# Performance work log

Hardware: AMD Instinct MI355X
Metric: run time of the kernel (lower is better)

The kernel has to match this reference:

```python
import jax, jax.numpy as jnp
import numpy as np

LN_EPS = 1e-12
NEG_INF = -1e9


def setup_inputs() -> dict:
    key = jax.random.key(0)
    ks = jax.random.split(key, 4)
    B, S, H = 8, 2048, 1024
    inputs = jax.random.normal(ks[0], (B, S, H), dtype=jnp.float32)
    masks = jnp.ones((B, S), dtype=jnp.int32)
    scale = 1.0 / np.sqrt(H)
    Wq = jax.random.normal(ks[1], (H, H), dtype=jnp.float32) * scale
    bq = jnp.zeros((H,), dtype=jnp.float32)
    Wk = jax.random.normal(ks[2], (H, H), dtype=jnp.float32) * scale
    bk = jnp.zeros((H,), dtype=jnp.float32)
    ln_gamma = jnp.ones((H,), dtype=jnp.float32)
    ln_beta = jnp.zeros((H,), dtype=jnp.float32)
    return {"inputs": inputs, "masks": masks, "Wq": Wq, "bq": bq,
            "Wk": Wk, "bk": bk, "ln_gamma": ln_gamma, "ln_beta": ln_beta}


def _layernorm(x, gamma, beta):
    mu = jnp.mean(x, axis=-1, keepdims=True)
    var = jnp.mean(jnp.square(x - mu), axis=-1, keepdims=True)
    return (x - mu) * jax.lax.rsqrt(var + LN_EPS) * gamma + beta


def reference(inputs, masks, Wq, bq, Wk, bk, ln_gamma, ln_beta):
    # inputs: [B,S,H]; masks: [B,S] (1 = keep key position)
    H = inputs.shape[-1]
    query = inputs @ Wq + bq                      # [B,S,H]
    key_ = inputs @ Wk + bk                       # [B,S,H]
    scores = jnp.einsum('bqh,bkh->bqk', query, key_) * (1.0 / jnp.sqrt(jnp.float32(H)))
    # logits_mask: invalid key positions get large negative logit
    scores = jnp.where(masks[:, None, :] != 0, scores, NEG_INF)
    probs = jax.nn.softmax(scores, axis=-1)       # [B,S,S]
    context = jnp.einsum('bqk,bkh->bqh', probs, inputs)  # value = raw inputs
    return _layernorm(inputs + context, ln_gamma, ln_beta)
```

## Files before the change

### kernel.cpp

```cpp
#include <hip/hip_runtime.h>
#include <stdint.h>
#include <stddef.h>

typedef _Float16 f16_t;
typedef _Float16 f16x8 __attribute__((ext_vector_type(8)));
typedef _Float16 f16x4 __attribute__((ext_vector_type(4)));
typedef float    f32x4 __attribute__((ext_vector_type(4)));

#define AS_G __attribute__((address_space(1)))
#define AS_L __attribute__((address_space(3)))

__device__ __forceinline__ void gload_lds16(const void* g, void* l) {
  __builtin_amdgcn_global_load_lds((const AS_G uint32_t*)g, (AS_L uint32_t*)l, 16, 0, 0);
}

#define LN_EPS 1e-12f
#define MASK_NEG -60000.0f

__global__ __launch_bounds__(256) void cast_f16_kernel(const float* __restrict__ in,
                                                       f16_t* __restrict__ out) {
  int i = blockIdx.x * 256 + threadIdx.x;
  float4 v = ((const float4*)in)[i];
  f16x4 o = {(f16_t)v.x, (f16_t)v.y, (f16_t)v.z, (f16_t)v.w};
  ((f16x4*)out)[i] = o;
}

__global__ __launch_bounds__(256) void transpose_f16_kernel(const float* __restrict__ in,
                                                            f16_t* __restrict__ out,
                                                            int R, int C) {
  __shared__ float tile[32][33];
  int b = blockIdx.z;
  const float* inb = in + (size_t)b * R * C;
  f16_t* outb = out + (size_t)b * R * C;
  int tx = threadIdx.x, ty = threadIdx.y;
  int c0 = blockIdx.x * 32, r0 = blockIdx.y * 32;
#pragma unroll
  for (int i = 0; i < 32; i += 8)
    tile[ty + i][tx] = inb[(size_t)(r0 + ty + i) * C + (c0 + tx)];
  __syncthreads();
#pragma unroll
  for (int i = 0; i < 32; i += 8)
    outb[(size_t)(c0 + ty + i) * R + (r0 + tx)] = (f16_t)tile[tx][ty + i];
}

__global__ __launch_bounds__(256) void gemm_bt_kernel(
    const f16_t* __restrict__ A, const f16_t* __restrict__ Bt, f16_t* __restrict__ C,
    const float* __restrict__ biasq, const float* __restrict__ biask,
    const int* __restrict__ mask,
    int lda, int ldb, int ldc, int K, float scale, int mode, int nhalf,
    size_t sA, size_t sB, size_t sC, size_t sMask) {
  __shared__ f16_t As[128 * 64];
  __shared__ f16_t Bs[128 * 64];

  const int tid = threadIdx.x;
  const int lane = tid & 63;
  const int wv = tid >> 6;
  const int m16 = lane & 15;
  const int quad = lane >> 4;
  const int wr = (wv >> 1) * 64;
  const int wc = (wv & 1) * 64;

  const f16_t* Ab = A + blockIdx.z * sA + (size_t)blockIdx.x * 128 * lda;
  const f16_t* Bb = Bt + blockIdx.z * sB + (size_t)blockIdx.y * 128 * ldb;

  const int lr8 = lane >> 3;
  const int ch8 = (lane & 7) ^ lr8;
  const f16_t* gA[4]; const f16_t* gB[4];
  f16_t* lA[4]; f16_t* lB[4];
#pragma unroll
  for (int j = 0; j < 4; ++j) {
    int row = wv * 32 + j * 8 + lr8;
    gA[j] = Ab + (size_t)row * lda + ch8 * 8;
    gB[j] = Bb + (size_t)row * ldb + ch8 * 8;
    lA[j] = &As[(wv * 32 + j * 8) * 64];
    lB[j] = &Bs[(wv * 32 + j * 8) * 64];
  }

  int aoff[4], boff[4], swz[2];
#pragma unroll
  for (int t = 0; t < 4; ++t) {
    aoff[t] = (wr + t * 16 + m16) * 64;
    boff[t] = (wc + t * 16 + m16) * 64;
  }
#pragma unroll
  for (int s = 0; s < 2; ++s)
    swz[s] = (((s << 2) | quad) ^ (m16 & 7)) * 8;

  f32x4 acc[4][4] = {};

  for (int k0 = 0; k0 < K; k0 += 64) {
#pragma unroll
    for (int j = 0; j < 4; ++j) {
      gload_lds16(gA[j] + k0, lA[j]);
      gload_lds16(gB[j] + k0, lB[j]);
    }
    __syncthreads();

#pragma unroll
    for (int s = 0; s < 2; ++s) {
      f16x8 af[4], bfr[4];
#pragma unroll
      for (int t = 0; t < 4; ++t) {
        af[t]  = *(const f16x8*)&As[aoff[t] + swz[s]];
        bfr[t] = *(const f16x8*)&Bs[boff[t] + swz[s]];
      }
#pragma unroll
      for (int rt = 0; rt < 4; ++rt)
#pragma unroll
        for (int ct = 0; ct < 4; ++ct)
          acc[rt][ct] = __builtin_amdgcn_mfma_f32_16x16x32_f16(af[rt], bfr[ct], acc[rt][ct], 0, 0, 0);
    }
    __syncthreads();
  }

  f16_t* Cb = C + blockIdx.z * sC;
  const int row0 = blockIdx.x * 128 + wr + quad * 4;
  const int col0 = blockIdx.y * 128 + wc + m16;
  if (mode == 0) {
#pragma unroll
    for (int ct = 0; ct < 4; ++ct) {
      int col = col0 + ct * 16;
      float bv = (col < nhalf) ? biasq[col] : biask[col - nhalf];
#pragma unroll
      for (int rt = 0; rt < 4; ++rt)
#pragma unroll
        for (int r = 0; r < 4; ++r)
          Cb[(size_t)(row0 + rt * 16 + r) * ldc + col] = (f16_t)(acc[rt][ct][r] + bv);
    }
  } else if (mode == 1) {
    const int* mp = mask + blockIdx.z * sMask;
#pragma unroll
    for (int ct = 0; ct < 4; ++ct) {
      int col = col0 + ct * 16;
      bool keep = (mp[col] != 0);
#pragma unroll
      for (int rt = 0; rt < 4; ++rt)
#pragma unroll
        for (int r = 0; r < 4; ++r) {
          float v = keep ? acc[rt][ct][r] * scale : MASK_NEG;
          Cb[(size_t)(row0 + rt * 16 + r) * ldc + col] = (f16_t)v;
        }
    }
  } else {
#pragma unroll
    for (int ct = 0; ct < 4; ++ct) {
      int col = col0 + ct * 16;
#pragma unroll
      for (int rt = 0; rt < 4; ++rt)
#pragma unroll
        for (int r = 0; r < 4; ++r)
          Cb[(size_t)(row0 + rt * 16 + r) * ldc + col] = (f16_t)acc[rt][ct][r];
    }
  }
}

__global__ __launch_bounds__(256) void softmax_kernel(f16_t* probs) {
  __shared__ float redm[4], reds[4];
  const int tid = threadIdx.x;
  f16_t* p = probs + (size_t)blockIdx.x * 2048;
  f16x8 v8 = ((const f16x8*)p)[tid];
  float v[8];
#pragma unroll
  for (int j = 0; j < 8; ++j) v[j] = (float)v8[j];
  float mx = v[0];
#pragma unroll
  for (int j = 1; j < 8; ++j) mx = fmaxf(mx, v[j]);
#pragma unroll
  for (int off = 32; off > 0; off >>= 1) mx = fmaxf(mx, __shfl_xor(mx, off, 64));
  if ((tid & 63) == 0) redm[tid >> 6] = mx;
  __syncthreads();
  mx = fmaxf(fmaxf(redm[0], redm[1]), fmaxf(redm[2], redm[3]));
  float e[8], s = 0.f;
#pragma unroll
  for (int j = 0; j < 8; ++j) { e[j] = __expf(v[j] - mx); s += e[j]; }
#pragma unroll
  for (int off = 32; off > 0; off >>= 1) s += __shfl_xor(s, off, 64);
  if ((tid & 63) == 0) reds[tid >> 6] = s;
  __syncthreads();
  s = reds[0] + reds[1] + reds[2] + reds[3];
  float inv = 1.0f / s;
  f16x8 o;
#pragma unroll
  for (int j = 0; j < 8; ++j) o[j] = (f16_t)(e[j] * inv);
  ((f16x8*)p)[tid] = o;
}

__global__ __launch_bounds__(256) void ln_kernel(const float* __restrict__ X,
                                                 const f16_t* __restrict__ Ctx,
                                                 const float* __restrict__ gamma,
                                                 const float* __restrict__ beta,
                                                 float* __restrict__ out) {
  __shared__ float r1[4], r2[4];
  const int tid = threadIdx.x;
  const size_t base = (size_t)blockIdx.x * 1024;
  float4 xv = ((const float4*)(X + base))[tid];
  f16x4 cv = ((const f16x4*)(Ctx + base))[tid];
  float v0 = xv.x + (float)cv[0];
  float v1 = xv.y + (float)cv[1];
  float v2 = xv.z + (float)cv[2];
  float v3 = xv.w + (float)cv[3];
  float s1 = v0 + v1 + v2 + v3;
  float s2 = v0 * v0 + v1 * v1 + v2 * v2 + v3 * v3;
#pragma unroll
  for (int off = 32; off > 0; off >>= 1) {
    s1 += __shfl_xor(s1, off, 64);
    s2 += __shfl_xor(s2, off, 64);
  }
  if ((tid & 63) == 0) { r1[tid >> 6] = s1; r2[tid >> 6] = s2; }
  __syncthreads();
  s1 = r1[0] + r1[1] + r1[2] + r1[3];
  s2 = r2[0] + r2[1] + r2[2] + r2[3];
  float mu = s1 * (1.0f / 1024.0f);
  float var = s2 * (1.0f / 1024.0f) - mu * mu;
  float rs = rsqrtf(fmaxf(var, 0.0f) + LN_EPS);
  float4 gv = ((const float4*)gamma)[tid];
  float4 bv = ((const float4*)beta)[tid];
  float4 o;
  o.x = (v0 - mu) * rs * gv.x + bv.x;
  o.y = (v1 - mu) * rs * gv.y + bv.y;
  o.z = (v2 - mu) * rs * gv.z + bv.z;
  o.w = (v3 - mu) * rs * gv.w + bv.w;
  ((float4*)(out + base))[tid] = o;
}

extern "C" void kernel_launch(void* const* d_in, const int* in_sizes, int n_in,
                              void* d_out, int out_size, void* d_ws, size_t ws_size,
                              hipStream_t stream) {
  const float* X     = (const float*)d_in[0];
  const int*   masks = (const int*)d_in[1];
  const float* Wq    = (const float*)d_in[2];
  const float* bq    = (const float*)d_in[3];
  const float* Wk    = (const float*)d_in[4];
  const float* bk    = (const float*)d_in[5];
  const float* gamma = (const float*)d_in[6];
  const float* beta  = (const float*)d_in[7];
  float* out = (float*)d_out;

  if (ws_size < 138412032u) return;
  char* ws = (char*)d_ws;
  f16_t* Xb    = (f16_t*)(ws + 0);
  f16_t* Xt    = (f16_t*)(ws + 33554432);
  f16_t* WqkT  = (f16_t*)(ws + 67108864);
  f16_t* QKb   = (f16_t*)(ws + 71303168);
  f16_t* Ctx = Xb;
  f16_t* probs = (f16_t*)d_out;

  const size_t SH = 2048u * 1024u;
  const size_t SS = 2048u * 2048u;
  const size_t HS = 1024u * 2048u;
  const size_t S2 = 2048u * 2048u;

  cast_f16_kernel<<<16384, 256, 0, stream>>>(X, Xb);
  transpose_f16_kernel<<<dim3(32, 64, 8), dim3(32, 8), 0, stream>>>(X, Xt, 2048, 1024);
  transpose_f16_kernel<<<dim3(32, 32, 1), dim3(32, 8), 0, stream>>>(Wq, WqkT, 1024, 1024);
  transpose_f16_kernel<<<dim3(32, 32, 1), dim3(32, 8), 0, stream>>>(Wk, WqkT + 1024 * 1024, 1024, 1024);

  gemm_bt_kernel<<<dim3(128, 16, 1), 256, 0, stream>>>(
      Xb, WqkT, QKb, bq, bk, nullptr,
      1024, 1024, 2048, 1024, 0.f, 0, 1024, 0, 0, 0, 0);

  gemm_bt_kernel<<<dim3(16, 16, 8), 256, 0, stream>>>(
      QKb, QKb + 1024, probs, nullptr, nullptr, masks,
      2048, 2048, 2048, 1024, 0.03125f, 1, 0, S2, S2, SS, 2048);

  softmax_kernel<<<16384, 256, 0, stream>>>(probs);

  gemm_bt_kernel<<<dim3(16, 8, 8), 256, 0, stream>>>(
      probs, Xt, Ctx, nullptr, nullptr, nullptr,
      2048, 2048, 1024, 2048, 0.f, 2, 0, SS, HS, SH, 0);

  ln_kernel<<<16384, 256, 0, stream>>>(X, Ctx, gamma, beta, out);
}
```

Measured before the change: 492.9 us.

## Fold Wq·Wkᵀ into one projection, fuse softmax into scores GEMM, double-buffer GEMM

The scores are rewritten algebraically as X(Wq Wkᵀ)Xᵀ plus rank-one bias terms. This replaces the 2048-wide QK projection with a single 1024-wide projection T = X·(Wq Wkᵀ) plus small bias vectors. The standalone softmax pass is removed: the score GEMM epilogue writes unnormalized exp values without max subtraction and per-block row partial sums. The normalization is then applied in the PV GEMM epilogue. The GEMM main loop now uses a K=32 double-buffered LDS pipeline with explicit waitcnt and barriers. Skipping the max subtraction relies on bounded logits for fp16/fp32 exp range, which is a numerical-robustness risk.

After: 504.4 us. 1.02x slower.

```diff
diff --git a/kernel.cpp b/kernel.cpp
--- a/kernel.cpp
+++ b/kernel.cpp
@@ -15,7 +15,6 @@
 }
 
 #define LN_EPS 1e-12f
-#define MASK_NEG -60000.0f
 
 __global__ __launch_bounds__(256) void cast_f16_kernel(const float* __restrict__ in,
                                                        f16_t* __restrict__ out) {
@@ -43,14 +42,59 @@
     outb[(size_t)(c0 + ty + i) * R + (r0 + tx)] = (f16_t)tile[tx][ty + i];
 }
 
+__global__ __launch_bounds__(256) void wvec_kernel(const float* __restrict__ Wq,
+                                                   const float* __restrict__ bq,
+                                                   const float* __restrict__ Wk,
+                                                   const float* __restrict__ bk,
+                                                   float* __restrict__ wqbk,
+                                                   float* __restrict__ wkbq,
+                                                   float* __restrict__ c0) {
+  __shared__ float red[4];
+  int bid = blockIdx.x, tid = threadIdx.x;
+  const float* rowp; const float* vecp; float* outp;
+  if (bid < 1024)      { rowp = Wq + (size_t)bid * 1024; vecp = bk; outp = wqbk + bid; }
+  else if (bid < 2048) { rowp = Wk + (size_t)(bid - 1024) * 1024; vecp = bq; outp = wkbq + (bid - 1024); }
+  else                 { rowp = bq; vecp = bk; outp = c0; }
+  float4 a = ((const float4*)rowp)[tid];
+  float4 b = ((const float4*)vecp)[tid];
+  float s = a.x * b.x + a.y * b.y + a.z * b.z + a.w * b.w;
+#pragma unroll
+  for (int off = 32; off > 0; off >>= 1) s += __shfl_xor(s, off, 64);
+  if ((tid & 63) == 0) red[tid >> 6] = s;
+  __syncthreads();
+  if (tid == 0) *outp = red[0] + red[1] + red[2] + red[3];
+}
+
+__global__ __launch_bounds__(256) void cqck_kernel(const float* __restrict__ X,
+                                                   const float* __restrict__ wqbk,
+                                                   const float* __restrict__ wkbq,
+                                                   float* __restrict__ cq,
+                                                   float* __restrict__ ck) {
+  __shared__ float r1[4], r2[4];
+  int m = blockIdx.x, tid = threadIdx.x;
+  float4 x = ((const float4*)(X + (size_t)m * 1024))[tid];
+  float4 a = ((const float4*)wqbk)[tid];
+  float4 b = ((const float4*)wkbq)[tid];
+  float s1 = x.x * a.x + x.y * a.y + x.z * a.z + x.w * a.w;
+  float s2 = x.x * b.x + x.y * b.y + x.z * b.z + x.w * b.w;
+#pragma unroll
+  for (int off = 32; off > 0; off >>= 1) { s1 += __shfl_xor(s1, off, 64); s2 += __shfl_xor(s2, off, 64); }
+  if ((tid & 63) == 0) { r1[tid >> 6] = s1; r2[tid >> 6] = s2; }
+  __syncthreads();
+  if (tid == 0) {
+    cq[m] = r1[0] + r1[1] + r1[2] + r1[3];
+    ck[m] = r2[0] + r2[1] + r2[2] + r2[3];
+  }
+}
+
 __global__ __launch_bounds__(256) void gemm_bt_kernel(
     const f16_t* __restrict__ A, const f16_t* __restrict__ Bt, f16_t* __restrict__ C,
-    const float* __restrict__ biasq, const float* __restrict__ biask,
-    const int* __restrict__ mask,
-    int lda, int ldb, int ldc, int K, float scale, int mode, int nhalf,
-    size_t sA, size_t sB, size_t sC, size_t sMask) {
-  __shared__ f16_t As[128 * 64];
-  __shared__ f16_t Bs[128 * 64];
+    const float* __restrict__ cq, const float* __restrict__ ck, const float* __restrict__ c0p,
+    const int* __restrict__ mask, const float* __restrict__ invl, float* __restrict__ lpart,
+    int lda, int ldb, int ldc, int K, float scale, int mode,
+    size_t sA, size_t sB, size_t sC) {
+  __shared__ f16_t As[2][128 * 32];
+  __shared__ f16_t Bs[2][128 * 32];
 
   const int tid = threadIdx.x;
   const int lane = tid & 63;
@@ -63,54 +107,58 @@
   const f16_t* Ab = A + blockIdx.z * sA + (size_t)blockIdx.x * 128 * lda;
   const f16_t* Bb = Bt + blockIdx.z * sB + (size_t)blockIdx.y * 128 * ldb;
 
-  const int lr8 = lane >> 3;
-  const int ch8 = (lane & 7) ^ lr8;
-  const f16_t* gA[4]; const f16_t* gB[4];
-  f16_t* lA[4]; f16_t* lB[4];
-#pragma unroll
-  for (int j = 0; j < 4; ++j) {
-    int row = wv * 32 + j * 8 + lr8;
-    gA[j] = Ab + (size_t)row * lda + ch8 * 8;
-    gB[j] = Bb + (size_t)row * ldb + ch8 * 8;
-    lA[j] = &As[(wv * 32 + j * 8) * 64];
-    lB[j] = &Bs[(wv * 32 + j * 8) * 64];
-  }
-
-  int aoff[4], boff[4], swz[2];
+  const int ch = ((lane & 3) ^ ((lane >> 3) & 3)) * 8;
+  const int r0 = wv * 32 + (lane >> 2);
+  const f16_t* gA0 = Ab + (size_t)r0 * lda + ch;
+  const f16_t* gA1 = Ab + (size_t)(r0 + 16) * lda + ch;
+  const f16_t* gB0 = Bb + (size_t)r0 * ldb + ch;
+  const f16_t* gB1 = Bb + (size_t)(r0 + 16) * ldb + ch;
+  const int ldsA0 = (wv * 32) * 32, ldsA1 = (wv * 32 + 16) * 32;
+
+  const int aslot = (quad ^ ((m16 >> 1) & 3)) * 8;
+  int aoff[4], boff[4];
 #pragma unroll
   for (int t = 0; t < 4; ++t) {
-    aoff[t] = (wr + t * 16 + m16) * 64;
-    boff[t] = (wc + t * 16 + m16) * 64;
-  }
-#pragma unroll
-  for (int s = 0; s < 2; ++s)
-    swz[s] = (((s << 2) | quad) ^ (m16 & 7)) * 8;
+    aoff[t] = (wr + t * 16 + m16) * 32 + aslot;
+    boff[t] = (wc + t * 16 + m16) * 32 + aslot;
+  }
 
   f32x4 acc[4][4] = {};
-
-  for (int k0 = 0; k0 < K; k0 += 64) {
-#pragma unroll
-    for (int j = 0; j < 4; ++j) {
-      gload_lds16(gA[j] + k0, lA[j]);
-      gload_lds16(gB[j] + k0, lB[j]);
+  const int nk = K >> 5;
+
+  gload_lds16(gA0, &As[0][ldsA0]);
+  gload_lds16(gA1, &As[0][ldsA1]);
+  gload_lds16(gB0, &Bs[0][ldsA0]);
+  gload_lds16(gB1, &Bs[0][ldsA1]);
+
+  int buf = 0;
+  for (int it = 0; it < nk; ++it) {
+    if (it + 1 < nk) {
+      const int k0 = (it + 1) << 5;
+      gload_lds16(gA0 + k0, &As[buf ^ 1][ldsA0]);
+      gload_lds16(gA1 + k0, &As[buf ^ 1][ldsA1]);
+      gload_lds16(gB0 + k0, &Bs[buf ^ 1][ldsA0]);
+      gload_lds16(gB1 + k0, &Bs[buf ^ 1][ldsA1]);
+      asm volatile("s_waitcnt vmcnt(4)" ::: "memory");
+    } else {
+      asm volatile("s_waitcnt vmcnt(0)" ::: "memory");
     }
-    __syncthreads();
-
-#pragma unroll
-    for (int s = 0; s < 2; ++s) {
-      f16x8 af[4], bfr[4];
-#pragma unroll
-      for (int t = 0; t < 4; ++t) {
-        af[t]  = *(const f16x8*)&As[aoff[t] + swz[s]];
-        bfr[t] = *(const f16x8*)&Bs[boff[t] + swz[s]];
-      }
-#pragma unroll
-      for (int rt = 0; rt < 4; ++rt)
-#pragma unroll
-        for (int ct = 0; ct < 4; ++ct)
-          acc[rt][ct] = __builtin_amdgcn_mfma_f32_16x16x32_f16(af[rt], bfr[ct], acc[rt][ct], 0, 0, 0);
+    asm volatile("s_barrier" ::: "memory");
+
+    f16x8 af[4], bfr[4];
+#pragma unroll
+    for (int t = 0; t < 4; ++t) {
+      af[t]  = *(const f16x8*)&As[buf][aoff[t]];
+      bfr[t] = *(const f16x8*)&Bs[buf][boff[t]];
     }
-    __syncthreads();
+#pragma unroll
+    for (int rt = 0; rt < 4; ++rt)
+#pragma unroll
+      for (int ct = 0; ct < 4; ++ct)
+        acc[rt][ct] = __builtin_amdgcn_mfma_f32_16x16x32_f16(af[rt], bfr[ct], acc[rt][ct], 0, 0, 0);
+
+    asm volatile("s_barrier" ::: "memory");
+    buf ^= 1;
   }
 
   f16_t* Cb = C + blockIdx.z * sC;
@@ -118,71 +166,73 @@
   const int col0 = blockIdx.y * 128 + wc + m16;
   if (mode == 0) {
 #pragma unroll
-    for (int ct = 0; ct < 4; ++ct) {
-      int col = col0 + ct * 16;
-      float bv = (col < nhalf) ? biasq[col] : biask[col - nhalf];
+    for (int ct = 0; ct < 4; ++ct)
 #pragma unroll
       for (int rt = 0; rt < 4; ++rt)
 #pragma unroll
         for (int r = 0; r < 4; ++r)
-          Cb[(size_t)(row0 + rt * 16 + r) * ldc + col] = (f16_t)(acc[rt][ct][r] + bv);
-    }
+          Cb[(size_t)(row0 + rt * 16 + r) * ldc + col0 + ct * 16] = (f16_t)acc[rt][ct][r];
   } else if (mode == 1) {
-    const int* mp = mask + blockIdx.z * sMask;
+    const int* mp = mask + blockIdx.z * 2048;
+    const size_t rowg0 = blockIdx.z * 2048 + row0;
+    const float c0 = *c0p;
+    float rsum[4][4];
+#pragma unroll
+    for (int rt = 0; rt < 4; ++rt)
+#pragma unroll
+      for (int r = 0; r < 4; ++r) rsum[rt][r] = 0.f;
 #pragma unroll
     for (int ct = 0; ct < 4; ++ct) {
       int col = col0 + ct * 16;
       bool keep = (mp[col] != 0);
+      float ckv = ck[blockIdx.z * 2048 + col];
 #pragma unroll
       for (int rt = 0; rt < 4; ++rt)
 #pragma unroll
         for (int r = 0; r < 4; ++r) {
-          float v = keep ? acc[rt][ct][r] * scale : MASK_NEG;
-          Cb[(size_t)(row0 + rt * 16 + r) * ldc + col] = (f16_t)v;
+          float cqv = cq[rowg0 + rt * 16 + r];
+          float p = keep ? __expf((acc[rt][ct][r] + cqv + ckv + c0) * scale) : 0.f;
+          rsum[rt][r] += p;
+          Cb[(size_t)(row0 + rt * 16 + r) * ldc + col] = (f16_t)p;
         }
     }
+    const int chunk = blockIdx.y * 2 + (wv & 1);
+#pragma unroll
+    for (int rt = 0; rt < 4; ++rt)
+#pragma unroll
+      for (int r = 0; r < 4; ++r) {
+        float v = rsum[rt][r];
+        v += __shfl_xor(v, 1, 16);
+        v += __shfl_xor(v, 2, 16);
+        v += __shfl_xor(v, 4, 16);
+        v += __shfl_xor(v, 8, 16);
+        if (m16 == 0) lpart[(rowg0 + rt * 16 + r) * 32 + chunk] = v;
+      }
   } else {
-#pragma unroll
-    for (int ct = 0; ct < 4; ++ct) {
-      int col = col0 + ct * 16;
-#pragma unroll
-      for (int rt = 0; rt < 4; ++rt)
-#pragma unroll
-        for (int r = 0; r < 4; ++r)
-          Cb[(size_t)(row0 + rt * 16 + r) * ldc + col] = (f16_t)acc[rt][ct][r];
-    }
-  }
-}
-
-__global__ __launch_bounds__(256) void softmax_kernel(f16_t* probs) {
-  __shared__ float redm[4], reds[4];
-  const int tid = threadIdx.x;
-  f16_t* p = probs + (size_t)blockIdx.x * 2048;
-  f16x8 v8 = ((const f16x8*)p)[tid];
-  float v[8];
-#pragma unroll
-  for (int j = 0; j < 8; ++j) v[j] = (float)v8[j];
-  float mx = v[0];
-#pragma unroll
-  for (int j = 1; j < 8; ++j) mx = fmaxf(mx, v[j]);
-#pragma unroll
-  for (int off = 32; off > 0; off >>= 1) mx = fmaxf(mx, __shfl_xor(mx, off, 64));
-  if ((tid & 63) == 0) redm[tid >> 6] = mx;
-  __syncthreads();
-  mx = fmaxf(fmaxf(redm[0], redm[1]), fmaxf(redm[2], redm[3]));
-  float e[8], s = 0.f;
-#pragma unroll
-  for (int j = 0; j < 8; ++j) { e[j] = __expf(v[j] - mx); s += e[j]; }
-#pragma unroll
-  for (int off = 32; off > 0; off >>= 1) s += __shfl_xor(s, off, 64);
-  if ((tid & 63) == 0) reds[tid >> 6] = s;
-  __syncthreads();
-  s = reds[0] + reds[1] + reds[2] + reds[3];
-  float inv = 1.0f / s;
-  f16x8 o;
-#pragma unroll
-  for (int j = 0; j < 8; ++j) o[j] = (f16_t)(e[j] * inv);
-  ((f16x8*)p)[tid] = o;
+    const size_t rowg0 = blockIdx.z * 2048 + row0;
+#pragma unroll
+    for (int rt = 0; rt < 4; ++rt)
+#pragma unroll
+      for (int r = 0; r < 4; ++r) {
+        float il = invl[rowg0 + rt * 16 + r];
+#pragma unroll
+        for (int ct = 0; ct < 4; ++ct)
+          Cb[(size_t)(row0 + rt * 16 + r) * ldc + col0 + ct * 16] = (f16_t)(acc[rt][ct][r] * il);
+      }
+  }
+}
+
+__global__ __launch_bounds__(256) void lreduce_kernel(const float* __restrict__ lpart,
+                                                      float* __restrict__ invl) {
+  int m = blockIdx.x * 256 + threadIdx.x;
+  const float4* p = (const float4*)(lpart + (size_t)m * 32);
+  float s = 0.f;
+#pragma unroll
+  for (int j = 0; j < 8; ++j) {
+    float4 v = p[j];
+    s += v.x + v.y + v.z + v.w;
+  }
+  invl[m] = 1.0f / fmaxf(s, 1e-30f);
 }
 
 __global__ __launch_bounds__(256) void ln_kernel(const float* __restrict__ X,
@@ -236,38 +286,52 @@
   const float* beta  = (const float*)d_in[7];
   float* out = (float*)d_out;
 
-  if (ws_size < 138412032u) return;
+  if (ws_size < 115343360u) return;
   char* ws = (char*)d_ws;
-  f16_t* Xb    = (f16_t*)(ws + 0);
-  f16_t* Xt    = (f16_t*)(ws + 33554432);
-  f16_t* WqkT  = (f16_t*)(ws + 67108864);
-  f16_t* QKb   = (f16_t*)(ws + 71303168);
-  f16_t* Ctx = Xb;
+  f16_t* Xb   = (f16_t*)(ws + 0);
+  f16_t* Xt   = (f16_t*)(ws + 33554432);
+  f16_t* T    = (f16_t*)(ws + 67108864);
+  f16_t* Wqf  = (f16_t*)(ws + 100663296);
+  f16_t* Wkf  = (f16_t*)(ws + 102760448);
+  f16_t* Wkq  = (f16_t*)(ws + 104857600);
+  float* lpart= (float*)(ws + 106954752);
+  float* cq   = (float*)(ws + 109051904);
+  float* ck   = (float*)(ws + 109117440);
+  float* invl = (float*)(ws + 109182976);
+  float* wqbk = (float*)(ws + 109248512);
+  float* wkbq = (float*)(ws + 109252608);
+  float* c0   = (float*)(ws + 109256704);
+  f16_t* Ctx  = Xb;
   f16_t* probs = (f16_t*)d_out;
 
   const size_t SH = 2048u * 1024u;
   const size_t SS = 2048u * 2048u;
   const size_t HS = 1024u * 2048u;
-  const size_t S2 = 2048u * 2048u;
 
   cast_f16_kernel<<<16384, 256, 0, stream>>>(X, Xb);
+  cast_f16_kernel<<<1024, 256, 0, stream>>>(Wq, Wqf);
+  cast_f16_kernel<<<1024, 256, 0, stream>>>(Wk, Wkf);
   transpose_f16_kernel<<<dim3(32, 64, 8), dim3(32, 8), 0, stream>>>(X, Xt, 2048, 1024);
-  transpose_f16_kernel<<<dim3(32, 32, 1), dim3(32, 8), 0, stream>>>(Wq, WqkT, 1024, 1024);
-  transpose_f16_kernel<<<dim3(32, 32, 1), dim3(32, 8), 0, stream>>>(Wk, WqkT + 1024 * 1024, 1024, 1024);
-
-  gemm_bt_kernel<<<dim3(128, 16, 1), 256, 0, stream>>>(
-      Xb, WqkT, QKb, bq, bk, nullptr,
-      1024, 1024, 2048, 1024, 0.f, 0, 1024, 0, 0, 0, 0);
+  wvec_kernel<<<2049, 256, 0, stream>>>(Wq, bq, Wk, bk, wqbk, wkbq, c0);
+  cqck_kernel<<<16384, 256, 0, stream>>>(X, wqbk, wkbq, cq, ck);
+
+  gemm_bt_kernel<<<dim3(8, 8, 1), 256, 0, stream>>>(
+      Wkf, Wqf, Wkq, nullptr, nullptr, nullptr, nullptr, nullptr, nullptr,
+      1024, 1024, 1024, 1024, 0.f, 0, 0, 0, 0);
+
+  gemm_bt_kernel<<<dim3(128, 8, 1), 256, 0, stream>>>(
+      Xb, Wkq, T, nullptr, nullptr, nullptr, nullptr, nullptr, nullptr,
+      1024, 1024, 1024, 1024, 0.f, 0, 0, 0, 0);
 
   gemm_bt_kernel<<<dim3(16, 16, 8), 256, 0, stream>>>(
-      QKb, QKb + 1024, probs, nullptr, nullptr, masks,
-      2048, 2048, 2048, 1024, 0.03125f, 1, 0, S2, S2, SS, 2048);
-
-  softmax_kernel<<<16384, 256, 0, stream>>>(probs);
+      T, Xb, probs, cq, ck, c0, masks, nullptr, lpart,
+      1024, 1024, 2048, 1024, 0.03125f, 1, SH, SH, SS);
+
+  lreduce_kernel<<<64, 256, 0, stream>>>(lpart, invl);
 
   gemm_bt_kernel<<<dim3(16, 8, 8), 256, 0, stream>>>(
-      probs, Xt, Ctx, nullptr, nullptr, nullptr,
-      2048, 2048, 1024, 2048, 0.f, 2, 0, SS, HS, SH, 0);
+      probs, Xt, Ctx, nullptr, nullptr, nullptr, nullptr, invl, nullptr,
+      2048, 2048, 1024, 2048, 0.f, 2, SS, HS, SH);
 
   ln_kernel<<<16384, 256, 0, stream>>>(X, Ctx, gamma, beta, out);
 }
```
